# Performance work log

Measured on AMD Instinct MI355X. Metric: run time of the kernel, lower is better.

## Reference

```python
import jax, jax.numpy as jnp
import numpy as np

N, E, H = 50000, 500000, 4
DIN, DH, DO, TD = 135, 128, 64, 9

def _ln(x, g, b):
    mu = jnp.mean(x, axis=-1, keepdims=True)
    v = jnp.var(x, axis=-1, keepdims=True)
    return (x - mu) / jnp.sqrt(v + 1e-5) * g + b

def _gat(x, src, dst, W, a_src, a_dst, b, n, heads, c):
    h = (x @ W).reshape(n, heads, c)                      # [N,H,C]
    es = jnp.sum(h * a_src, -1)                           # [N,H]
    ed = jnp.sum(h * a_dst, -1)
    e = jax.nn.leaky_relu(es[src] + ed[dst], 0.2)         # [E,H]
    m = jax.ops.segment_max(e, dst, num_segments=n)       # segment softmax over dst
    ex = jnp.exp(e - m[dst])
    den = jax.ops.segment_sum(ex, dst, num_segments=n)
    alpha = ex / (den[dst] + 1e-16)
    out = jax.ops.segment_sum(h[src] * alpha[..., None], dst, num_segments=n)
    return jnp.mean(out, axis=1) + b                      # concat=False -> head mean

def setup_inputs() -> dict:
    key = jax.random.key(0)
    ks = jax.random.split(key, 32)
    rn = lambda i, shape: jax.random.normal(ks[i], shape, jnp.float32) * 0.05
    inp = {}
    inp['x'] = jax.random.normal(ks[0], (N, DIN), jnp.float32)
    inp['edge_index'] = jax.random.randint(ks[1], (2, E), 0, N, jnp.int32)
    inp['edge_attr'] = jnp.ones((E, 1), jnp.float32)
    inp['W_in'] = rn(2, (DIN, DH)); inp['b_in'] = jnp.zeros((DH,), jnp.float32)
    inp['g1W'] = rn(3, (DH, H * DH)); inp['g1as'] = rn(4, (H, DH)); inp['g1ad'] = rn(5, (H, DH)); inp['g1b'] = jnp.zeros((DH,), jnp.float32)
    inp['g2W'] = rn(6, (DH, H * DH)); inp['g2as'] = rn(7, (H, DH)); inp['g2ad'] = rn(8, (H, DH)); inp['g2b'] = jnp.zeros((DH,), jnp.float32)
    inp['g3W'] = rn(9, (DH, H * DO)); inp['g3as'] = rn(10, (H, DO)); inp['g3ad'] = rn(11, (H, DO)); inp['g3b'] = jnp.zeros((DO,), jnp.float32)
    inp['r1W'] = rn(12, (DH, DH)); inp['r1b'] = jnp.zeros((DH,), jnp.float32)
    inp['r2W'] = rn(13, (DH, DH)); inp['r2b'] = jnp.zeros((DH,), jnp.float32)
    inp['r3W'] = rn(14, (DH, DO)); inp['r3b'] = jnp.zeros((DO,), jnp.float32)
    inp['n1g'] = jnp.ones((DH,), jnp.float32); inp['n1b'] = jnp.zeros((DH,), jnp.float32)
    inp['n2g'] = jnp.ones((DH,), jnp.float32); inp['n2b'] = jnp.zeros((DH,), jnp.float32)
    inp['n3g'] = jnp.ones((DO,), jnp.float32); inp['n3b'] = jnp.zeros((DO,), jnp.float32)
    inp['tw'] = jnp.float32(0.3)
    inp['c1W'] = rn(15, (DO, DO)); inp['c1b'] = jnp.zeros((DO,), jnp.float32)
    inp['clg'] = jnp.ones((DO,), jnp.float32); inp['clb'] = jnp.zeros((DO,), jnp.float32)
    inp['c2W'] = rn(16, (DO, 2)); inp['c2b'] = jnp.zeros((2,), jnp.float32)
    return inp

def reference(x, edge_index, edge_attr, W_in, b_in, g1W, g1as, g1ad, g1b,
              g2W, g2as, g2ad, g2b, g3W, g3as, g3ad, g3b,
              r1W, r1b, r2W, r2b, r3W, r3b,
              n1g, n1b, n2g, n2b, n3g, n3b, tw,
              c1W, c1b, clg, clb, c2W, c2b):
    n = x.shape[0]
    src0, dst0 = edge_index[0], edge_index[1]
    loop = jnp.arange(n, dtype=edge_index.dtype)          # GATConv add_self_loops=True
    src = jnp.concatenate([src0, loop])
    dst = jnp.concatenate([dst0, loop])
    # vectorized temporal cosine similarity over original edges
    t = x[:, -TD:]
    ti, tj = t[src0], t[dst0]
    nrm = jnp.maximum(jnp.linalg.norm(ti, axis=-1), 1e-8) * jnp.maximum(jnp.linalg.norm(tj, axis=-1), 1e-8)
    sim = jnp.sum(ti * tj, -1) / nrm
    scale = 1.0 + 0.1 * jnp.mean(1.0 + tw * sim)
    h = x @ W_in + b_in
    id1 = h
    h = _gat(h, src, dst, g1W, g1as, g1ad, g1b, n, H, DH) * scale
    h = _ln(jax.nn.relu(h) + id1 @ r1W + r1b, n1g, n1b)
    id2 = h
    h = _gat(h, src, dst, g2W, g2as, g2ad, g2b, n, H, DH) * scale
    h = _ln(jax.nn.relu(h) + id2 @ r2W + r2b, n2g, n2b)
    id3 = h
    h = _gat(h, src, dst, g3W, g3as, g3ad, g3b, n, H, DO)
    h = _ln(jax.nn.relu(h) + id3 @ r3W + r3b, n3g, n3b)
    ego = h[0:1]
    z = jax.nn.relu(ego @ c1W + c1b)
    z = _ln(z, clg, clb)
    return z @ c2W + c2b
```

## Files before the change

### kernel.cpp

```cpp
#include <hip/hip_runtime.h>

#define AGENT __HIP_MEMORY_SCOPE_AGENT

constexpr int TD = 9, TDP = 12, DIN = 135;
constexpr int CAPD = 64;
constexpr int CAP3 = 256, CAP2 = 1024, CAP1 = 4096;
constexpr int NBM = 512;
constexpr int LSTRIDE = 32;
constexpr int NGRP = 16;
constexpr int GSZ = NBM / NGRP;
constexpr int NSET = 8;
constexpr int NLINE = 64;
constexpr int PB = 8;

struct P {
  const float* x; const int* src; const int* dst; int N; int E;
  const float *W_in,*b_in,*g1W,*g1as,*g1ad,*g1b,*g2W,*g2as,*g2ad,*g2b,*g3W,*g3as,*g3ad,*g3b;
  const float *r1W,*r1b,*r2W,*r2b,*r3W,*r3b,*n1g,*n1b,*n2g,*n2b,*n3g,*n3b;
  const float *tw,*c1W,*c1b,*clg,*clb,*c2W,*c2b;
  float* tp;
  int *deg, *bk;
  int *m3,*m2,*m1,*list3,*list2,*list1,*cnts;
  int *barc,*barr,*barg;
  float *h0,*hh1,*es1,*ed1,*h1,*hh2,*es2,*ed2,*h2,*hh3,*es3,*ed3,*h3;
  float* dout;
};

__device__ __forceinline__ float lrelu(float v) { return v >= 0.f ? v : 0.2f * v; }

__device__ __forceinline__ void stg(float* pp, float v) { __hip_atomic_store(pp, v, __ATOMIC_RELAXED, AGENT); }
__device__ __forceinline__ void stg(int* pp, int v)   { __hip_atomic_store(pp, v, __ATOMIC_RELAXED, AGENT); }

__device__ __forceinline__ void claim_node(int v, int* __restrict__ m, int* __restrict__ list,
                                           int* __restrict__ cnt, int cap) {
  if (atomicCAS(&m[v], -1, -2) == -1) {
    int pos = atomicAdd(cnt, 1);
    if (pos < cap) { stg(&list[pos], v); stg(&m[v], pos); } else { stg(&m[v], -3); }
  }
}

__device__ __forceinline__ void mid_barrier(const P& p, int& lgen, int* amroot_s) {
  __syncthreads();
  int g = lgen + 1;
  if (threadIdx.x == 0) {
    *amroot_s = 0;
    int* gc = &p.barc[(((g & (NSET - 1)) * NGRP) + (blockIdx.x & (NGRP - 1))) * LSTRIDE];
    if (__hip_atomic_fetch_add(gc, 1, __ATOMIC_RELAXED, AGENT) == GSZ - 1) {
      int* rc = &p.barr[(g & (NSET - 1)) * LSTRIDE];
      if (__hip_atomic_fetch_add(rc, 1, __ATOMIC_RELAXED, AGENT) == NGRP - 1) *amroot_s = 1;
    }
  }
  __syncthreads();
  if (*amroot_s) {
    if (threadIdx.x < NLINE)
      __hip_atomic_store(&p.barg[threadIdx.x * LSTRIDE], g, __ATOMIC_RELAXED, AGENT);
  } else if (threadIdx.x == 0) {
    int* line = &p.barg[(blockIdx.x & (NLINE - 1)) * LSTRIDE];
    while (__hip_atomic_load(line, __ATOMIC_RELAXED, AGENT) < g)
      __builtin_amdgcn_s_sleep(8);
  }
  __syncthreads();
  lgen = g;
}

__global__ void k_prep(P p) {
  int gt = blockIdx.x * blockDim.x + threadIdx.x;
  int GT = gridDim.x * blockDim.x;
  int n3 = 3 * p.N;
  int4* mv = (int4*)p.m3;
  int4 neg = make_int4(-1, -1, -1, -1);
  int nv = n3 >> 2;
  for (int i = gt; i < nv; i += GT) mv[i] = neg;
  for (int i = (nv << 2) + gt; i < n3; i += GT) p.m3[i] = -1;
  int4* dv = (int4*)p.deg;
  int4 z4 = make_int4(0, 0, 0, 0);
  int ndv = p.N >> 2;
  for (int i = gt; i < ndv; i += GT) dv[i] = z4;
  for (int i = (ndv << 2) + gt; i < p.N; i += GT) p.deg[i] = 0;
  if (gt < 64) p.cnts[gt] = 0;
  for (int i = gt; i < NSET * NGRP * LSTRIDE; i += GT) p.barc[i] = 0;
  for (int i = gt; i < NSET * LSTRIDE; i += GT) p.barr[i] = 0;
  for (int i = gt; i < NLINE * LSTRIDE; i += GT) p.barg[i] = 0;
  int total = p.N * TDP;
  for (int i = gt; i < total; i += GT) {
    int v = i / TDP, k = i - v * TDP;
    p.tp[i] = (k < TD) ? p.x[(size_t)v * DIN + (DIN - TD) + k] : 0.f;
  }
}

__global__ void k_scan(P p) {
  __shared__ float wred[4];
  int tid = threadIdx.x;
  int gt = blockIdx.x * blockDim.x + tid, GT = gridDim.x * blockDim.x;
  if (gt == 0) claim_node(0, p.m3, p.list3, &p.cnts[0], CAP3);
  const float4* t4 = (const float4*)p.tp;
  float local = 0.f;
  auto edge_proc = [&](int s, int d) {
    int slot = atomicAdd(&p.deg[d], 1);
    if (slot < CAPD) p.bk[(size_t)d * CAPD + slot] = s;
    if (d == 0) claim_node(s, p.m3, p.list3, &p.cnts[0], CAP3);
    float4 a0 = t4[s * 3], a1 = t4[s * 3 + 1], a2 = t4[s * 3 + 2];
    float4 b0 = t4[d * 3], b1 = t4[d * 3 + 1], b2 = t4[d * 3 + 2];
    float dot = a0.x*b0.x + a0.y*b0.y + a0.z*b0.z + a0.w*b0.w
              + a1.x*b1.x + a1.y*b1.y + a1.z*b1.z + a1.w*b1.w
              + a2.x*b2.x;
    float na = a0.x*a0.x + a0.y*a0.y + a0.z*a0.z + a0.w*a0.w
             + a1.x*a1.x + a1.y*a1.y + a1.z*a1.z + a1.w*a1.w
             + a2.x*a2.x;
    float nb = b0.x*b0.x + b0.y*b0.y + b0.z*b0.z + b0.w*b0.w
             + b1.x*b1.x + b1.y*b1.y + b1.z*b1.z + b1.w*b1.w
             + b2.x*b2.x;
    local += dot / (fmaxf(sqrtf(na), 1e-8f) * fmaxf(sqrtf(nb), 1e-8f));
  };
  int nq4 = p.E >> 2;
  const int4* s4p = (const int4*)p.src;
  const int4* d4p = (const int4*)p.dst;
  for (int q = gt; q < nq4; q += GT) {
    int4 s4 = s4p[q], d4 = d4p[q];
    edge_proc(s4.x, d4.x); edge_proc(s4.y, d4.y); edge_proc(s4.z, d4.z); edge_proc(s4.w, d4.w);
  }
  for (int e = (nq4 << 2) + gt; e < p.E; e += GT) edge_proc(p.src[e], p.dst[e]);
  for (int off = 32; off > 0; off >>= 1) local += __shfl_down(local, off, 64);
  if ((tid & 63) == 0) wred[tid >> 6] = local;
  __syncthreads();
  if (tid == 0) atomicAdd((float*)&p.cnts[8], wred[0] + wred[1] + wred[2] + wred[3]);
}

template <int C, int ONEXT>
__device__ void gat_dev(const P& p, int nq, const int* lst, const int* mPrev,
                        const float* hh, const float* es, const float* ed, const float* hres,
                        const float* gb, const float* rW, const float* rb,
                        const float* ng, const float* nbv, float scale,
                        float* hout, const float* Wn, const float* avn, const float* bvn,
                        float* hhn, float* esn, float* edn,
                        float* elog, int* eposs, float* ev_s, float* sh,
                        float* hres_s, float* shln, float* psn, float* pdn, float* sc2) {
  const int Wd = 4 * C, R = Wd / 256;
  int tid = threadIdx.x;
  for (int q = blockIdx.x; q < nq; q += gridDim.x) {
    int v = lst[q];
    int sp = mPrev[v];
    int nb = min(p.deg[v], CAPD);
    for (int j = tid; j < nb; j += 256) {
      int pu = mPrev[p.bk[(size_t)v * CAPD + j]];
      eposs[j] = pu;
      const float* ep = &es[(size_t)pu * 4];
      elog[0 * CAPD + j] = ep[0]; elog[1 * CAPD + j] = ep[1];
      elog[2 * CAPD + j] = ep[2]; elog[3 * CAPD + j] = ep[3];
    }
    if (tid < 4) { ev_s[tid] = es[(size_t)sp * 4 + tid]; ev_s[4 + tid] = ed[(size_t)sp * 4 + tid]; }
    for (int k = tid; k < 128; k += 256) hres_s[k] = hres[(size_t)sp * 128 + k];
    __syncthreads();
#pragma unroll
    for (int r = 0; r < R; r++) {
      int w = r * 256 + tid, a = w / C;
      float edv = ev_s[4 + a];
      float eself = lrelu(ev_s[a] + edv);
      float mx = eself;
      for (int j = 0; j < nb; j++) mx = fmaxf(mx, lrelu(elog[a * CAPD + j] + edv));
      float den = __expf(eself - mx);
      for (int j = 0; j < nb; j++) den += __expf(lrelu(elog[a * CAPD + j] + edv) - mx);
      float rden = 1.f / (den + 1e-16f);
      float s = __expf(eself - mx) * rden * hh[(size_t)sp * Wd + w];
      for (int j = 0; j < nb; j++)
        s += __expf(lrelu(elog[a * CAPD + j] + edv) - mx) * rden * hh[(size_t)eposs[j] * Wd + w];
      sh[w] = s;
    }
    __syncthreads();
    float val = 0.f;
    if (tid < C) {
      float g = 0.25f * (sh[tid] + sh[C + tid] + sh[2 * C + tid] + sh[3 * C + tid]) + gb[tid];
      g *= scale;
      g = fmaxf(g, 0.f);
      float rr = rb[tid];
      for (int k = 0; k < 128; k++) rr += hres_s[k] * rW[(size_t)k * C + tid];
      val = g + rr;
      shln[tid] = val;
    }
    __syncthreads();
    if (tid == 0) {
      float s1 = 0.f, s2 = 0.f;
      for (int k = 0; k < C; k++) { float u = shln[k]; s1 += u; s2 += u * u; }
      float mu = s1 / (float)C;
      sc2[0] = mu;
      sc2[1] = rsqrtf(fmaxf(s2 / (float)C - mu * mu, 0.f) + 1e-5f);
    }
    __syncthreads();
    if (tid < C) {
      float o = (val - sc2[0]) * sc2[1] * ng[tid] + nbv[tid];
      stg(&hout[(size_t)q * C + tid], o);
      shln[tid] = o;
    }
    __syncthreads();
    if (ONEXT > 0) {
      for (int j = tid; j < ONEXT; j += 256) {
        float a2 = 0.f;
        for (int k = 0; k < C; k++) a2 += shln[k] * Wn[(size_t)k * ONEXT + j];
        stg(&hhn[(size_t)q * ONEXT + j], a2);
        psn[j] = a2 * avn[j]; pdn[j] = a2 * bvn[j];
      }
      __syncthreads();
      if (tid < 8) {
        const int CN = ONEXT / 4; int a = tid & 3;
        const float* pr = (tid < 4) ? psn : pdn;
        float s = 0.f;
        for (int cc = 0; cc < CN; cc++) s += pr[a * CN + cc];
        stg(&(tid < 4 ? esn : edn)[(size_t)q * 4 + a], s);
      }
      __syncthreads();
    }
  }
}

__global__ __launch_bounds__(256, 2) void k_mid(P p) {
  __shared__ float xs8[PB][DIN];
  __shared__ float hs8[PB][128];
  __shared__ float psn[512], pdn[512];
  __shared__ int   vid8[PB];
  __shared__ float elog[4 * CAPD];
  __shared__ int   eposs[CAPD];
  __shared__ float ev_s[8], sc2[2];
  __shared__ float sh[512], hres_s[128], shln[128];
  __shared__ float zcl[64];
  __shared__ int   amroot_s;

  int tid = threadIdx.x, bid = blockIdx.x;
  int lgen = 0;
  float scale = 1.1f + 0.1f * p.tw[0] *
      __int_as_float(__hip_atomic_load(&p.cnts[8], __ATOMIC_RELAXED, AGENT)) / (float)p.E;

  {
    int c3 = min(__hip_atomic_load(&p.cnts[0], __ATOMIC_RELAXED, AGENT), CAP3);
    for (int q = bid; q < c3; q += NBM) {
      int v = p.list3[q];
      if (tid == 0) claim_node(v, p.m2, p.list2, &p.cnts[1], CAP2);
      int nb = min(p.deg[v], CAPD);
      for (int j = tid; j < nb; j += 256)
        claim_node(p.bk[(size_t)v * CAPD + j], p.m2, p.list2, &p.cnts[1], CAP2);
    }
  }
  mid_barrier(p, lgen, &amroot_s);

  {
    int c2 = min(__hip_atomic_load(&p.cnts[1], __ATOMIC_RELAXED, AGENT), CAP2);
    for (int q = bid; q < c2; q += NBM) {
      int v = p.list2[q];
      if (tid == 0) claim_node(v, p.m1, p.list1, &p.cnts[2], CAP1);
      int nb = min(p.deg[v], CAPD);
      for (int j = tid; j < nb; j += 256)
        claim_node(p.bk[(size_t)v * CAPD + j], p.m1, p.list1, &p.cnts[2], CAP1);
    }
  }
  mid_barrier(p, lgen, &amroot_s);

  {
    int c1 = min(__hip_atomic_load(&p.cnts[2], __ATOMIC_RELAXED, AGENT), CAP1);
    int ngp = (c1 + PB - 1) / PB;
    for (int g = bid; g < ngp; g += NBM) {
      int base = g * PB, nn = min(PB, c1 - base);
      if (tid < nn) vid8[tid] = p.list1[base + tid];
      __syncthreads();
      for (int idx = tid; idx < nn * DIN; idx += 256) {
        int u = idx / DIN, k = idx - u * DIN;
        xs8[u][k] = p.x[(size_t)vid8[u] * DIN + k];
      }
      __syncthreads();
      if (tid < 128) {
        float a[PB]; float bi = p.b_in[tid];
#pragma unroll
        for (int u = 0; u < PB; u++) a[u] = bi;
        for (int k = 0; k < DIN; k++) {
          float w = p.W_in[(size_t)k * 128 + tid];
#pragma unroll
          for (int u = 0; u < PB; u++) a[u] += xs8[u][k] * w;
        }
#pragma unroll
        for (int u = 0; u < PB; u++) {
          hs8[u][tid] = a[u];
          if (u < nn) stg(&p.h0[(size_t)(base + u) * 128 + tid], a[u]);
        }
      }
      __syncthreads();
      float bsv[2][PB];
#pragma unroll
      for (int jj = 0; jj < 2; jj++) {
        int j = jj * 256 + tid;
        float b[PB];
#pragma unroll
        for (int u = 0; u < PB; u++) b[u] = 0.f;
        for (int k = 0; k < 128; k++) {
          float w = p.g1W[(size_t)k * 512 + j];
#pragma unroll
          for (int u = 0; u < PB; u++) b[u] += hs8[u][k] * w;
        }
#pragma unroll
        for (int u = 0; u < PB; u++) {
          bsv[jj][u] = b[u];
          if (u < nn) stg(&p.hh1[(size_t)(base + u) * 512 + j], b[u]);
        }
      }
      for (int u = 0; u < nn; u++) {
#pragma unroll
        for (int jj = 0; jj < 2; jj++) {
          int j = jj * 256 + tid;
          psn[j] = bsv[jj][u] * p.g1as[j];
          pdn[j] = bsv[jj][u] * p.g1ad[j];
        }
        __syncthreads();
        if (tid < 8) {
          int a = tid & 3;
          const float* pr = (tid < 4) ? psn : pdn;
          float s = 0.f;
          for (int cc = 0; cc < 128; cc++) s += pr[a * 128 + cc];
          stg(&(tid < 4 ? p.es1 : p.ed1)[(size_t)(base + u) * 4 + a], s);
        }
        __syncthreads();
      }
    }
  }
  mid_barrier(p, lgen, &amroot_s);

  {
    int c2 = min(__hip_atomic_load(&p.cnts[1], __ATOMIC_RELAXED, AGENT), CAP2);
    gat_dev<128, 512>(p, c2, p.list2, p.m1, p.hh1, p.es1, p.ed1, p.h0,
                      p.g1b, p.r1W, p.r1b, p.n1g, p.n1b, scale,
                      p.h1, p.g2W, p.g2as, p.g2ad, p.hh2, p.es2, p.ed2,
                      elog, eposs, ev_s, sh, hres_s, shln, psn, pdn, sc2);
  }
  mid_barrier(p, lgen, &amroot_s);

  {
    int c3 = min(__hip_atomic_load(&p.cnts[0], __ATOMIC_RELAXED, AGENT), CAP3);
    gat_dev<128, 256>(p, c3, p.list3, p.m2, p.hh2, p.es2, p.ed2, p.h1,
                      p.g2b, p.r2W, p.r2b, p.n2g, p.n2b, scale,
                      p.h2, p.g3W, p.g3as, p.g3ad, p.hh3, p.es3, p.ed3,
                      elog, eposs, ev_s, sh, hres_s, shln, psn, pdn, sc2);
  }
  mid_barrier(p, lgen, &amroot_s);

  if (bid == 0) {
    int zero = 0;
    gat_dev<64, 0>(p, 1, &zero , p.m3,
                   p.hh3, p.es3, p.ed3, p.h2,
                   p.g3b, p.r3W, p.r3b, p.n3g, p.n3b, 1.f,
                   p.h3, nullptr, nullptr, nullptr, nullptr, nullptr, nullptr,
                   elog, eposs, ev_s, sh, hres_s, shln, psn, pdn, sc2);
    if (tid < 64) {
      float az = p.c1b[tid];
      for (int k = 0; k < 64; k++) az += shln[k] * p.c1W[k * 64 + tid];
      zcl[tid] = fmaxf(az, 0.f);
    }
    __syncthreads();
    if (tid == 0) {
      float s1 = 0.f, s2 = 0.f;
      for (int k = 0; k < 64; k++) { float u = zcl[k]; s1 += u; s2 += u * u; }
      float mu = s1 / 64.f;
      float rstd = rsqrtf(fmaxf(s2 / 64.f - mu * mu, 0.f) + 1e-5f);
      float o0 = p.c2b[0], o1 = p.c2b[1];
      for (int k = 0; k < 64; k++) {
        float zn = (zcl[k] - mu) * rstd * p.clg[k] + p.clb[k];
        o0 += zn * p.c2W[k * 2 + 0];
        o1 += zn * p.c2W[k * 2 + 1];
      }
      p.dout[0] = o0; p.dout[1] = o1;
    }
  }
}

extern "C" void kernel_launch(void* const* d_in, const int* in_sizes, int n_in,
                              void* d_out, int out_size, void* d_ws, size_t ws_size,
                              hipStream_t stream) {
  P p;
  p.x = (const float*)d_in[0];
  const int* ei = (const int*)d_in[1];
  p.N = in_sizes[0] / DIN;
  p.E = in_sizes[1] / 2;
  p.src = ei; p.dst = ei + p.E;
  p.W_in = (const float*)d_in[3]; p.b_in = (const float*)d_in[4];
  p.g1W = (const float*)d_in[5]; p.g1as = (const float*)d_in[6]; p.g1ad = (const float*)d_in[7]; p.g1b = (const float*)d_in[8];
  p.g2W = (const float*)d_in[9]; p.g2as = (const float*)d_in[10]; p.g2ad = (const float*)d_in[11]; p.g2b = (const float*)d_in[12];
  p.g3W = (const float*)d_in[13]; p.g3as = (const float*)d_in[14]; p.g3ad = (const float*)d_in[15]; p.g3b = (const float*)d_in[16];
  p.r1W = (const float*)d_in[17]; p.r1b = (const float*)d_in[18];
  p.r2W = (const float*)d_in[19]; p.r2b = (const float*)d_in[20];
  p.r3W = (const float*)d_in[21]; p.r3b = (const float*)d_in[22];
  p.n1g = (const float*)d_in[23]; p.n1b = (const float*)d_in[24];
  p.n2g = (const float*)d_in[25]; p.n2b = (const float*)d_in[26];
  p.n3g = (const float*)d_in[27]; p.n3b = (const float*)d_in[28];
  p.tw  = (const float*)d_in[29];
  p.c1W = (const float*)d_in[30]; p.c1b = (const float*)d_in[31];
  p.clg = (const float*)d_in[32]; p.clb = (const float*)d_in[33];
  p.c2W = (const float*)d_in[34]; p.c2b = (const float*)d_in[35];
  p.dout = (float*)d_out;

  char* B = (char*)d_ws;
  size_t off = 0;
  auto take = [&](size_t nbytes) -> char* {
    char* r = B + off;
    off += (nbytes + 255) & ~(size_t)255;
    return r;
  };
  p.cnts  = (int*)take(256);
  p.barc  = (int*)take((size_t)NSET * NGRP * LSTRIDE * 4);
  p.barr  = (int*)take((size_t)NSET * LSTRIDE * 4);
  p.barg  = (int*)take((size_t)NLINE * LSTRIDE * 4);
  p.m3    = (int*)take((size_t)3 * p.N * 4);
  p.m2 = p.m3 + p.N; p.m1 = p.m2 + p.N;
  p.tp    = (float*)take((size_t)p.N * TDP * 4);
  p.deg   = (int*)take((size_t)p.N * 4);
  p.bk    = (int*)take((size_t)p.N * CAPD * 4);
  p.list3 = (int*)take(CAP3 * 4);
  p.list2 = (int*)take(CAP2 * 4);
  p.list1 = (int*)take(CAP1 * 4);
  p.h0    = (float*)take((size_t)CAP1 * 128 * 4);
  p.hh1   = (float*)take((size_t)CAP1 * 512 * 4);
  p.es1   = (float*)take((size_t)CAP1 * 16);
  p.ed1   = (float*)take((size_t)CAP1 * 16);
  p.h1    = (float*)take((size_t)CAP2 * 128 * 4);
  p.hh2   = (float*)take((size_t)CAP2 * 512 * 4);
  p.es2   = (float*)take((size_t)CAP2 * 16);
  p.ed2   = (float*)take((size_t)CAP2 * 16);
  p.h2    = (float*)take((size_t)CAP3 * 128 * 4);
  p.hh3   = (float*)take((size_t)CAP3 * 256 * 4);
  p.es3   = (float*)take((size_t)CAP3 * 16);
  p.ed3   = (float*)take((size_t)CAP3 * 16);
  p.h3    = (float*)take(64 * 4);

  k_prep<<<1024, 256, 0, stream>>>(p);
  k_scan<<<1024, 256, 0, stream>>>(p);
  k_mid<<<NBM, 256, 0, stream>>>(p);
}
```

Baseline: 134.9 us.

## Fuse layer-1 input projection into per-node GAT1 with online softmax

Removes the separate level-1 frontier expansion and the precompute of h0/hh1/es/ed for the 2-hop set, together with two grid barriers. Instead, each GAT1 node block recomputes the input and GAT1 projections for its own neighbours in chunks of 16 and aggregates them with an online (running-max) softmax. This trades duplicate projection work for neighbours shared between nodes against fewer global barriers, less global memory traffic and no list1 claiming atomics. Shared memory grows considerably because of the chunk buffers, which may reduce occupancy.

```diff
diff --git a/kernel.cpp b/kernel.cpp
--- a/kernel.cpp
+++ b/kernel.cpp
@@ -4,14 +4,13 @@
 
 constexpr int TD = 9, TDP = 12, DIN = 135;
 constexpr int CAPD = 64;
-constexpr int CAP3 = 256, CAP2 = 1024, CAP1 = 4096;
+constexpr int CAP3 = 256, CAP2 = 1024;
 constexpr int NBM = 512;
 constexpr int LSTRIDE = 32;
-constexpr int NGRP = 16;
-constexpr int GSZ = NBM / NGRP;
+constexpr int NGRP = 16, GSZ = NBM / NGRP;
 constexpr int NSET = 8;
 constexpr int NLINE = 64;
-constexpr int PB = 8;
+constexpr int UB = 16;
 
 struct P {
   const float* x; const int* src; const int* dst; int N; int E;
@@ -20,9 +19,9 @@
   const float *tw,*c1W,*c1b,*clg,*clb,*c2W,*c2b;
   float* tp;
   int *deg, *bk;
-  int *m3,*m2,*m1,*list3,*list2,*list1,*cnts;
+  int *m3,*m2,*list3,*list2,*cnts;
   int *barc,*barr,*barg;
-  float *h0,*hh1,*es1,*ed1,*h1,*hh2,*es2,*ed2,*h2,*hh3,*es3,*ed3,*h3;
+  float *h1,*hh2,*es2,*ed2,*h2,*hh3,*es3,*ed3,*h3;
   float* dout;
 };
 
@@ -66,12 +65,12 @@
 __global__ void k_prep(P p) {
   int gt = blockIdx.x * blockDim.x + threadIdx.x;
   int GT = gridDim.x * blockDim.x;
-  int n3 = 3 * p.N;
+  int n2 = 2 * p.N;
   int4* mv = (int4*)p.m3;
   int4 neg = make_int4(-1, -1, -1, -1);
-  int nv = n3 >> 2;
+  int nv = n2 >> 2;
   for (int i = gt; i < nv; i += GT) mv[i] = neg;
-  for (int i = (nv << 2) + gt; i < n3; i += GT) p.m3[i] = -1;
+  for (int i = (nv << 2) + gt; i < n2; i += GT) p.m3[i] = -1;
   int4* dv = (int4*)p.deg;
   int4 z4 = make_int4(0, 0, 0, 0);
   int ndv = p.N >> 2;
@@ -126,239 +125,313 @@
   if (tid == 0) atomicAdd((float*)&p.cnts[8], wred[0] + wred[1] + wred[2] + wred[3]);
 }
 
+struct MidSmem {
+  float xs[UB][DIN];
+  float h0c[UB][128];
+  float hh1c[UB][512];
+  float h0self[128];
+  float sh[512];
+  float psn[512], pdn[512];
+  float pes[UB][4][4], ped[UB][4][4];
+  float esc[UB][4], edc[UB][4];
+  float wch[UB][4];
+  float mden_m[4], mden_d[4], ffac[4], edv[4];
+  int   uid[UB];
+  float elog[4 * CAPD];
+  int   eposs[CAPD];
+  float hres_s[128], shln[128];
+  float ev_s[8], sc2[2], zcl[64];
+  int   amroot;
+};
+
+__device__ void gat1_fused(const P& p, int q, float scale, MidSmem& s) {
+  int tid = threadIdx.x;
+  int v = p.list2[q];
+  int nb = min(p.deg[v], CAPD);
+  int np = nb + 1;
+  if (tid < 4) { s.mden_m[tid] = -1e30f; s.mden_d[tid] = 0.f; }
+  float agg0 = 0.f, agg1 = 0.f;
+  int a0 = tid >> 7, a1 = a0 + 2;
+  for (int c0 = 0; c0 < np; c0 += UB) {
+    int cnt = min(UB, np - c0);
+    if (tid < UB)
+      s.uid[tid] = (tid < cnt) ? ((c0 + tid == 0) ? v : p.bk[(size_t)v * CAPD + (c0 + tid - 1)]) : 0;
+    __syncthreads();
+    for (int idx = tid; idx < UB * DIN; idx += 256) {
+      int u = idx / DIN, k = idx - u * DIN;
+      s.xs[u][k] = (u < cnt) ? p.x[(size_t)s.uid[u] * DIN + k] : 0.f;
+    }
+    __syncthreads();
+    if (tid < 128) {
+      float a[UB];
+      float bi = p.b_in[tid];
+#pragma unroll
+      for (int u = 0; u < UB; u++) a[u] = bi;
+      for (int k = 0; k < DIN; k++) {
+        float w = p.W_in[(size_t)k * 128 + tid];
+#pragma unroll
+        for (int u = 0; u < UB; u++) a[u] += s.xs[u][k] * w;
+      }
+#pragma unroll
+      for (int u = 0; u < UB; u++) s.h0c[u][tid] = a[u];
+    }
+    __syncthreads();
+    if (c0 == 0 && tid < 128) s.h0self[tid] = s.h0c[0][tid];
+    {
+      float b0[UB], b1[UB];
+#pragma unroll
+      for (int u = 0; u < UB; u++) { b0[u] = 0.f; b1[u] = 0.f; }
+      for (int k = 0; k < 128; k++) {
+        float w0 = p.g1W[(size_t)k * 512 + tid];
+        float w1 = p.g1W[(size_t)k * 512 + tid + 256];
+#pragma unroll
+        for (int u = 0; u < UB; u++) { b0[u] += s.h0c[u][k] * w0; b1[u] += s.h0c[u][k] * w1; }
+      }
+#pragma unroll
+      for (int u = 0; u < UB; u++) { s.hh1c[u][tid] = b0[u]; s.hh1c[u][tid + 256] = b1[u]; }
+    }
+    __syncthreads();
+    {
+      int u = tid >> 4, aa = (tid >> 2) & 3, part = tid & 3;
+      float se = 0.f, sd = 0.f;
+      int base = aa * 128 + part * 32;
+      for (int c = 0; c < 32; c++) {
+        float hv = s.hh1c[u][base + c];
+        se += hv * p.g1as[base + c];
+        sd += hv * p.g1ad[base + c];
+      }
+      s.pes[u][aa][part] = se; s.ped[u][aa][part] = sd;
+    }
+    __syncthreads();
+    if (tid < UB * 4) {
+      int u = tid >> 2, aa = tid & 3;
+      s.esc[u][aa] = s.pes[u][aa][0] + s.pes[u][aa][1] + s.pes[u][aa][2] + s.pes[u][aa][3];
+      s.edc[u][aa] = s.ped[u][aa][0] + s.ped[u][aa][1] + s.ped[u][aa][2] + s.ped[u][aa][3];
+    }
+    __syncthreads();
+    if (tid < 4) {
+      int aa = tid;
+      if (c0 == 0) s.edv[aa] = s.edc[0][aa];
+      float ev = s.edv[aa];
+      float mold = s.mden_m[aa];
+      float mc = mold;
+      for (int u = 0; u < cnt; u++) {
+        float e = lrelu(s.esc[u][aa] + ev);
+        s.wch[u][aa] = e;
+        if (e > mc) mc = e;
+      }
+      float f = __expf(mold - mc);
+      float dn = s.mden_d[aa] * f;
+      for (int u = 0; u < cnt; u++) {
+        float w = __expf(s.wch[u][aa] - mc);
+        s.wch[u][aa] = w;
+        dn += w;
+      }
+      for (int u = cnt; u < UB; u++) s.wch[u][aa] = 0.f;
+      s.mden_m[aa] = mc; s.mden_d[aa] = dn; s.ffac[aa] = f;
+    }
+    __syncthreads();
+    {
+      float f0 = s.ffac[a0], f1 = s.ffac[a1];
+      float s0 = 0.f, s1 = 0.f;
+#pragma unroll
+      for (int u = 0; u < UB; u++) {
+        s0 += s.wch[u][a0] * s.hh1c[u][tid];
+        s1 += s.wch[u][a1] * s.hh1c[u][tid + 256];
+      }
+      agg0 = agg0 * f0 + s0;
+      agg1 = agg1 * f1 + s1;
+    }
+    __syncthreads();
+  }
+  s.sh[tid]       = agg0 / (s.mden_d[a0] + 1e-16f);
+  s.sh[tid + 256] = agg1 / (s.mden_d[a1] + 1e-16f);
+  __syncthreads();
+  float val = 0.f;
+  if (tid < 128) {
+    float g = 0.25f * (s.sh[tid] + s.sh[128 + tid] + s.sh[256 + tid] + s.sh[384 + tid]) + p.g1b[tid];
+    g *= scale;
+    g = fmaxf(g, 0.f);
+    float rr = p.r1b[tid];
+    for (int k = 0; k < 128; k++) rr += s.h0self[k] * p.r1W[(size_t)k * 128 + tid];
+    val = g + rr;
+    s.shln[tid] = val;
+  }
+  __syncthreads();
+  if (tid == 0) {
+    float s1 = 0.f, s2 = 0.f;
+    for (int k = 0; k < 128; k++) { float u = s.shln[k]; s1 += u; s2 += u * u; }
+    float mu = s1 / 128.f;
+    s.sc2[0] = mu;
+    s.sc2[1] = rsqrtf(fmaxf(s2 / 128.f - mu * mu, 0.f) + 1e-5f);
+  }
+  __syncthreads();
+  if (tid < 128) {
+    float o = (val - s.sc2[0]) * s.sc2[1] * p.n1g[tid] + p.n1b[tid];
+    stg(&p.h1[(size_t)q * 128 + tid], o);
+    s.shln[tid] = o;
+  }
+  __syncthreads();
+  {
+    float a2_0 = 0.f, a2_1 = 0.f;
+    for (int k = 0; k < 128; k++) {
+      float hv = s.shln[k];
+      a2_0 += hv * p.g2W[(size_t)k * 512 + tid];
+      a2_1 += hv * p.g2W[(size_t)k * 512 + tid + 256];
+    }
+    stg(&p.hh2[(size_t)q * 512 + tid], a2_0);
+    stg(&p.hh2[(size_t)q * 512 + tid + 256], a2_1);
+    s.psn[tid] = a2_0 * p.g2as[tid];
+    s.psn[tid + 256] = a2_1 * p.g2as[tid + 256];
+    s.pdn[tid] = a2_0 * p.g2ad[tid];
+    s.pdn[tid + 256] = a2_1 * p.g2ad[tid + 256];
+  }
+  __syncthreads();
+  if (tid < 16) {
+    int aa = tid >> 2, part = tid & 3;
+    float se = 0.f, sd = 0.f;
+    int base = aa * 128 + part * 32;
+    for (int c = 0; c < 32; c++) { se += s.psn[base + c]; sd += s.pdn[base + c]; }
+    s.pes[0][aa][part] = se; s.ped[0][aa][part] = sd;
+  }
+  __syncthreads();
+  if (tid < 4) {
+    stg(&p.es2[(size_t)q * 4 + tid],
+        s.pes[0][tid][0] + s.pes[0][tid][1] + s.pes[0][tid][2] + s.pes[0][tid][3]);
+    stg(&p.ed2[(size_t)q * 4 + tid],
+        s.ped[0][tid][0] + s.ped[0][tid][1] + s.ped[0][tid][2] + s.ped[0][tid][3]);
+  }
+  __syncthreads();
+}
+
 template <int C, int ONEXT>
-__device__ void gat_dev(const P& p, int nq, const int* lst, const int* mPrev,
-                        const float* hh, const float* es, const float* ed, const float* hres,
-                        const float* gb, const float* rW, const float* rb,
-                        const float* ng, const float* nbv, float scale,
-                        float* hout, const float* Wn, const float* avn, const float* bvn,
-                        float* hhn, float* esn, float* edn,
-                        float* elog, int* eposs, float* ev_s, float* sh,
-                        float* hres_s, float* shln, float* psn, float* pdn, float* sc2) {
+__device__ void gat_q(const P& p, int q, const int* lst, const int* mPrev,
+                      const float* hh, const float* es, const float* ed, const float* hres,
+                      const float* gb, const float* rW, const float* rb,
+                      const float* ng, const float* nbv, float scale,
+                      float* hout, const float* Wn, const float* avn, const float* bvn,
+                      float* hhn, float* esn, float* edn, MidSmem& s) {
   const int Wd = 4 * C, R = Wd / 256;
   int tid = threadIdx.x;
-  for (int q = blockIdx.x; q < nq; q += gridDim.x) {
-    int v = lst[q];
-    int sp = mPrev[v];
-    int nb = min(p.deg[v], CAPD);
-    for (int j = tid; j < nb; j += 256) {
-      int pu = mPrev[p.bk[(size_t)v * CAPD + j]];
-      eposs[j] = pu;
-      const float* ep = &es[(size_t)pu * 4];
-      elog[0 * CAPD + j] = ep[0]; elog[1 * CAPD + j] = ep[1];
-      elog[2 * CAPD + j] = ep[2]; elog[3 * CAPD + j] = ep[3];
-    }
-    if (tid < 4) { ev_s[tid] = es[(size_t)sp * 4 + tid]; ev_s[4 + tid] = ed[(size_t)sp * 4 + tid]; }
-    for (int k = tid; k < 128; k += 256) hres_s[k] = hres[(size_t)sp * 128 + k];
-    __syncthreads();
-#pragma unroll
-    for (int r = 0; r < R; r++) {
-      int w = r * 256 + tid, a = w / C;
-      float edv = ev_s[4 + a];
-      float eself = lrelu(ev_s[a] + edv);
-      float mx = eself;
-      for (int j = 0; j < nb; j++) mx = fmaxf(mx, lrelu(elog[a * CAPD + j] + edv));
-      float den = __expf(eself - mx);
-      for (int j = 0; j < nb; j++) den += __expf(lrelu(elog[a * CAPD + j] + edv) - mx);
-      float rden = 1.f / (den + 1e-16f);
-      float s = __expf(eself - mx) * rden * hh[(size_t)sp * Wd + w];
-      for (int j = 0; j < nb; j++)
-        s += __expf(lrelu(elog[a * CAPD + j] + edv) - mx) * rden * hh[(size_t)eposs[j] * Wd + w];
-      sh[w] = s;
-    }
-    __syncthreads();
-    float val = 0.f;
-    if (tid < C) {
-      float g = 0.25f * (sh[tid] + sh[C + tid] + sh[2 * C + tid] + sh[3 * C + tid]) + gb[tid];
-      g *= scale;
-      g = fmaxf(g, 0.f);
-      float rr = rb[tid];
-      for (int k = 0; k < 128; k++) rr += hres_s[k] * rW[(size_t)k * C + tid];
-      val = g + rr;
-      shln[tid] = val;
-    }
-    __syncthreads();
-    if (tid == 0) {
-      float s1 = 0.f, s2 = 0.f;
-      for (int k = 0; k < C; k++) { float u = shln[k]; s1 += u; s2 += u * u; }
-      float mu = s1 / (float)C;
-      sc2[0] = mu;
-      sc2[1] = rsqrtf(fmaxf(s2 / (float)C - mu * mu, 0.f) + 1e-5f);
-    }
-    __syncthreads();
-    if (tid < C) {
-      float o = (val - sc2[0]) * sc2[1] * ng[tid] + nbv[tid];
-      stg(&hout[(size_t)q * C + tid], o);
-      shln[tid] = o;
-    }
-    __syncthreads();
-    if (ONEXT > 0) {
-      for (int j = tid; j < ONEXT; j += 256) {
-        float a2 = 0.f;
-        for (int k = 0; k < C; k++) a2 += shln[k] * Wn[(size_t)k * ONEXT + j];
-        stg(&hhn[(size_t)q * ONEXT + j], a2);
-        psn[j] = a2 * avn[j]; pdn[j] = a2 * bvn[j];
-      }
-      __syncthreads();
-      if (tid < 8) {
-        const int CN = ONEXT / 4; int a = tid & 3;
-        const float* pr = (tid < 4) ? psn : pdn;
-        float s = 0.f;
-        for (int cc = 0; cc < CN; cc++) s += pr[a * CN + cc];
-        stg(&(tid < 4 ? esn : edn)[(size_t)q * 4 + a], s);
-      }
-      __syncthreads();
-    }
-  }
+  int v = lst[q];
+  int sp = mPrev[v];
+  int nb = min(p.deg[v], CAPD);
+  for (int j = tid; j < nb; j += 256) {
+    int pu = mPrev[p.bk[(size_t)v * CAPD + j]];
+    s.eposs[j] = pu;
+    const float* ep = &es[(size_t)pu * 4];
+    s.elog[0 * CAPD + j] = ep[0]; s.elog[1 * CAPD + j] = ep[1];
+    s.elog[2 * CAPD + j] = ep[2]; s.elog[3 * CAPD + j] = ep[3];
+  }
+  if (tid < 4) { s.ev_s[tid] = es[(size_t)sp * 4 + tid]; s.ev_s[4 + tid] = ed[(size_t)sp * 4 + tid]; }
+  for (int k = tid; k < 128; k += 256) s.hres_s[k] = hres[(size_t)sp * 128 + k];
+  __syncthreads();
+#pragma unroll
+  for (int r = 0; r < R; r++) {
+    int w = r * 256 + tid, a = w / C;
+    float edv = s.ev_s[4 + a];
+    float eself = lrelu(s.ev_s[a] + edv);
+    float mx = eself;
+    for (int j = 0; j < nb; j++) mx = fmaxf(mx, lrelu(s.elog[a * CAPD + j] + edv));
+    float den = __expf(eself - mx);
+    for (int j = 0; j < nb; j++) den += __expf(lrelu(s.elog[a * CAPD + j] + edv) - mx);
+    float rden = 1.f / (den + 1e-16f);
+    float sv = __expf(eself - mx) * rden * hh[(size_t)sp * Wd + w];
+    for (int j = 0; j < nb; j++)
+      sv += __expf(lrelu(s.elog[a * CAPD + j] + edv) - mx) * rden * hh[(size_t)s.eposs[j] * Wd + w];
+    s.sh[w] = sv;
+  }
+  __syncthreads();
+  float val = 0.f;
+  if (tid < C) {
+    float g = 0.25f * (s.sh[tid] + s.sh[C + tid] + s.sh[2 * C + tid] + s.sh[3 * C + tid]) + gb[tid];
+    g *= scale;
+    g = fmaxf(g, 0.f);
+    float rr = rb[tid];
+    for (int k = 0; k < 128; k++) rr += s.hres_s[k] * rW[(size_t)k * C + tid];
+    val = g + rr;
+    s.shln[tid] = val;
+  }
+  __syncthreads();
+  if (tid == 0) {
+    float s1 = 0.f, s2 = 0.f;
+    for (int k = 0; k < C; k++) { float u = s.shln[k]; s1 += u; s2 += u * u; }
+    float mu = s1 / (float)C;
+    s.sc2[0] = mu;
+    s.sc2[1] = rsqrtf(fmaxf(s2 / (float)C - mu * mu, 0.f) + 1e-5f);
+  }
+  __syncthreads();
+  if (tid < C) {
+    float o = (val - s.sc2[0]) * s.sc2[1] * ng[tid] + nbv[tid];
+    stg(&hout[(size_t)q * C + tid], o);
+    s.shln[tid] = o;
+  }
+  __syncthreads();
+  if (ONEXT > 0) {
+    for (int j = tid; j < ONEXT; j += 256) {
+      float a2 = 0.f;
+      for (int k = 0; k < C; k++) a2 += s.shln[k] * Wn[(size_t)k * ONEXT + j];
+      stg(&hhn[(size_t)q * ONEXT + j], a2);
+      s.psn[j] = a2 * avn[j]; s.pdn[j] = a2 * bvn[j];
+    }
+    __syncthreads();
+    if (tid < 8) {
+      const int CN = ONEXT / 4; int a = tid & 3;
+      const float* pr = (tid < 4) ? s.psn : s.pdn;
+      float sv = 0.f;
+      for (int cc = 0; cc < CN; cc++) sv += pr[a * CN + cc];
+      stg(&(tid < 4 ? esn : edn)[(size_t)q * 4 + a], sv);
+    }
+  }
+  __syncthreads();
 }
 
 __global__ __launch_bounds__(256, 2) void k_mid(P p) {
-  __shared__ float xs8[PB][DIN];
-  __shared__ float hs8[PB][128];
-  __shared__ float psn[512], pdn[512];
-  __shared__ int   vid8[PB];
-  __shared__ float elog[4 * CAPD];
-  __shared__ int   eposs[CAPD];
-  __shared__ float ev_s[8], sc2[2];
-  __shared__ float sh[512], hres_s[128], shln[128];
-  __shared__ float zcl[64];
-  __shared__ int   amroot_s;
-
+  __shared__ MidSmem s;
   int tid = threadIdx.x, bid = blockIdx.x;
   int lgen = 0;
   float scale = 1.1f + 0.1f * p.tw[0] *
       __int_as_float(__hip_atomic_load(&p.cnts[8], __ATOMIC_RELAXED, AGENT)) / (float)p.E;
 
-  {
-    int c3 = min(__hip_atomic_load(&p.cnts[0], __ATOMIC_RELAXED, AGENT), CAP3);
-    for (int q = bid; q < c3; q += NBM) {
-      int v = p.list3[q];
-      if (tid == 0) claim_node(v, p.m2, p.list2, &p.cnts[1], CAP2);
-      int nb = min(p.deg[v], CAPD);
-      for (int j = tid; j < nb; j += 256)
-        claim_node(p.bk[(size_t)v * CAPD + j], p.m2, p.list2, &p.cnts[1], CAP2);
-    }
-  }
-  mid_barrier(p, lgen, &amroot_s);
-
-  {
-    int c2 = min(__hip_atomic_load(&p.cnts[1], __ATOMIC_RELAXED, AGENT), CAP2);
-    for (int q = bid; q < c2; q += NBM) {
-      int v = p.list2[q];
-      if (tid == 0) claim_node(v, p.m1, p.list1, &p.cnts[2], CAP1);
-      int nb = min(p.deg[v], CAPD);
-      for (int j = tid; j < nb; j += 256)
-        claim_node(p.bk[(size_t)v * CAPD + j], p.m1, p.list1, &p.cnts[2], CAP1);
-    }
-  }
-  mid_barrier(p, lgen, &amroot_s);
-
-  {
-    int c1 = min(__hip_atomic_load(&p.cnts[2], __ATOMIC_RELAXED, AGENT), CAP1);
-    int ngp = (c1 + PB - 1) / PB;
-    for (int g = bid; g < ngp; g += NBM) {
-      int base = g * PB, nn = min(PB, c1 - base);
-      if (tid < nn) vid8[tid] = p.list1[base + tid];
-      __syncthreads();
-      for (int idx = tid; idx < nn * DIN; idx += 256) {
-        int u = idx / DIN, k = idx - u * DIN;
-        xs8[u][k] = p.x[(size_t)vid8[u] * DIN + k];
-      }
-      __syncthreads();
-      if (tid < 128) {
-        float a[PB]; float bi = p.b_in[tid];
-#pragma unroll
-        for (int u = 0; u < PB; u++) a[u] = bi;
-        for (int k = 0; k < DIN; k++) {
-          float w = p.W_in[(size_t)k * 128 + tid];
-#pragma unroll
-          for (int u = 0; u < PB; u++) a[u] += xs8[u][k] * w;
-        }
-#pragma unroll
-        for (int u = 0; u < PB; u++) {
-          hs8[u][tid] = a[u];
-          if (u < nn) stg(&p.h0[(size_t)(base + u) * 128 + tid], a[u]);
-        }
-      }
-      __syncthreads();
-      float bsv[2][PB];
-#pragma unroll
-      for (int jj = 0; jj < 2; jj++) {
-        int j = jj * 256 + tid;
-        float b[PB];
-#pragma unroll
-        for (int u = 0; u < PB; u++) b[u] = 0.f;
-        for (int k = 0; k < 128; k++) {
-          float w = p.g1W[(size_t)k * 512 + j];
-#pragma unroll
-          for (int u = 0; u < PB; u++) b[u] += hs8[u][k] * w;
-        }
-#pragma unroll
-        for (int u = 0; u < PB; u++) {
-          bsv[jj][u] = b[u];
-          if (u < nn) stg(&p.hh1[(size_t)(base + u) * 512 + j], b[u]);
-        }
-      }
-      for (int u = 0; u < nn; u++) {
-#pragma unroll
-        for (int jj = 0; jj < 2; jj++) {
-          int j = jj * 256 + tid;
-          psn[j] = bsv[jj][u] * p.g1as[j];
-          pdn[j] = bsv[jj][u] * p.g1ad[j];
-        }
-        __syncthreads();
-        if (tid < 8) {
-          int a = tid & 3;
-          const float* pr = (tid < 4) ? psn : pdn;
-          float s = 0.f;
-          for (int cc = 0; cc < 128; cc++) s += pr[a * 128 + cc];
-          stg(&(tid < 4 ? p.es1 : p.ed1)[(size_t)(base + u) * 4 + a], s);
-        }
-        __syncthreads();
-      }
-    }
-  }
-  mid_barrier(p, lgen, &amroot_s);
-
-  {
-    int c2 = min(__hip_atomic_load(&p.cnts[1], __ATOMIC_RELAXED, AGENT), CAP2);
-    gat_dev<128, 512>(p, c2, p.list2, p.m1, p.hh1, p.es1, p.ed1, p.h0,
-                      p.g1b, p.r1W, p.r1b, p.n1g, p.n1b, scale,
-                      p.h1, p.g2W, p.g2as, p.g2ad, p.hh2, p.es2, p.ed2,
-                      elog, eposs, ev_s, sh, hres_s, shln, psn, pdn, sc2);
-  }
-  mid_barrier(p, lgen, &amroot_s);
-
-  {
-    int c3 = min(__hip_atomic_load(&p.cnts[0], __ATOMIC_RELAXED, AGENT), CAP3);
-    gat_dev<128, 256>(p, c3, p.list3, p.m2, p.hh2, p.es2, p.ed2, p.h1,
-                      p.g2b, p.r2W, p.r2b, p.n2g, p.n2b, scale,
-                      p.h2, p.g3W, p.g3as, p.g3ad, p.hh3, p.es3, p.ed3,
-                      elog, eposs, ev_s, sh, hres_s, shln, psn, pdn, sc2);
-  }
-  mid_barrier(p, lgen, &amroot_s);
+  int c3 = min(__hip_atomic_load(&p.cnts[0], __ATOMIC_RELAXED, AGENT), CAP3);
+  for (int q = bid; q < c3; q += NBM) {
+    int v = p.list3[q];
+    if (tid == 0) claim_node(v, p.m2, p.list2, &p.cnts[1], CAP2);
+    int nb = min(p.deg[v], CAPD);
+    for (int j = tid; j < nb; j += 256)
+      claim_node(p.bk[(size_t)v * CAPD + j], p.m2, p.list2, &p.cnts[1], CAP2);
+  }
+  mid_barrier(p, lgen, &s.amroot);
+
+  int c2 = min(__hip_atomic_load(&p.cnts[1], __ATOMIC_RELAXED, AGENT), CAP2);
+  for (int q = bid; q < c2; q += NBM) gat1_fused(p, q, scale, s);
+  mid_barrier(p, lgen, &s.amroot);
+
+  for (int q = bid; q < c3; q += NBM)
+    gat_q<128, 256>(p, q, p.list3, p.m2, p.hh2, p.es2, p.ed2, p.h1,
+                    p.g2b, p.r2W, p.r2b, p.n2g, p.n2b, scale,
+                    p.h2, p.g3W, p.g3as, p.g3ad, p.hh3, p.es3, p.ed3, s);
+  mid_barrier(p, lgen, &s.amroot);
 
   if (bid == 0) {
     int zero = 0;
-    gat_dev<64, 0>(p, 1, &zero , p.m3,
-                   p.hh3, p.es3, p.ed3, p.h2,
-                   p.g3b, p.r3W, p.r3b, p.n3g, p.n3b, 1.f,
-                   p.h3, nullptr, nullptr, nullptr, nullptr, nullptr, nullptr,
-                   elog, eposs, ev_s, sh, hres_s, shln, psn, pdn, sc2);
+    gat_q<64, 0>(p, 0, &zero, p.m3, p.hh3, p.es3, p.ed3, p.h2,
+                 p.g3b, p.r3W, p.r3b, p.n3g, p.n3b, 1.f,
+                 p.h3, nullptr, nullptr, nullptr, nullptr, nullptr, nullptr, s);
     if (tid < 64) {
       float az = p.c1b[tid];
-      for (int k = 0; k < 64; k++) az += shln[k] * p.c1W[k * 64 + tid];
-      zcl[tid] = fmaxf(az, 0.f);
+      for (int k = 0; k < 64; k++) az += s.shln[k] * p.c1W[k * 64 + tid];
+      s.zcl[tid] = fmaxf(az, 0.f);
     }
     __syncthreads();
     if (tid == 0) {
       float s1 = 0.f, s2 = 0.f;
-      for (int k = 0; k < 64; k++) { float u = zcl[k]; s1 += u; s2 += u * u; }
+      for (int k = 0; k < 64; k++) { float u = s.zcl[k]; s1 += u; s2 += u * u; }
       float mu = s1 / 64.f;
       float rstd = rsqrtf(fmaxf(s2 / 64.f - mu * mu, 0.f) + 1e-5f);
       float o0 = p.c2b[0], o1 = p.c2b[1];
       for (int k = 0; k < 64; k++) {
-        float zn = (zcl[k] - mu) * rstd * p.clg[k] + p.clb[k];
+        float zn = (s.zcl[k] - mu) * rstd * p.clg[k] + p.clb[k];
         o0 += zn * p.c2W[k * 2 + 0];
         o1 += zn * p.c2W[k * 2 + 1];
       }
@@ -403,18 +476,13 @@
   p.barc  = (int*)take((size_t)NSET * NGRP * LSTRIDE * 4);
   p.barr  = (int*)take((size_t)NSET * LSTRIDE * 4);
   p.barg  = (int*)take((size_t)NLINE * LSTRIDE * 4);
-  p.m3    = (int*)take((size_t)3 * p.N * 4);
-  p.m2 = p.m3 + p.N; p.m1 = p.m2 + p.N;
+  p.m3    = (int*)take((size_t)2 * p.N * 4);
+  p.m2 = p.m3 + p.N;
   p.tp    = (float*)take((size_t)p.N * TDP * 4);
   p.deg   = (int*)take((size_t)p.N * 4);
   p.bk    = (int*)take((size_t)p.N * CAPD * 4);
   p.list3 = (int*)take(CAP3 * 4);
   p.list2 = (int*)take(CAP2 * 4);
-  p.list1 = (int*)take(CAP1 * 4);
-  p.h0    = (float*)take((size_t)CAP1 * 128 * 4);
-  p.hh1   = (float*)take((size_t)CAP1 * 512 * 4);
-  p.es1   = (float*)take((size_t)CAP1 * 16);
-  p.ed1   = (float*)take((size_t)CAP1 * 16);
   p.h1    = (float*)take((size_t)CAP2 * 128 * 4);
   p.hh2   = (float*)take((size_t)CAP2 * 512 * 4);
   p.es2   = (float*)take((size_t)CAP2 * 16);
```

Result: slower. 280.3 us (+107.7%).
